# Kernel optimization log

Hardware: AMD Instinct MI355X
Metric: run time of the kernel (lower is better)

The kernel has to match this reference:

```python
import jax, jax.numpy as jnp
import numpy as np

DIM = 1024
NUM_HEADS = 16
HEAD_DIM = DIM // NUM_HEADS
SCALE = HEAD_DIM ** (-0.5)


def setup_inputs() -> dict:
    key = jax.random.key(0)
    ks = jax.random.split(key, 5)
    B, L, D = 2, 2048, DIM
    x = jax.random.normal(ks[0], (B, L, D), dtype=jnp.float32)
    # torch nn.Linear init scale ~ U(-1/sqrt(fan_in), 1/sqrt(fan_in)); use small normals
    s = 1.0 / np.sqrt(D)
    qkv_w = jax.random.uniform(ks[1], (3 * D, D), minval=-s, maxval=s, dtype=jnp.float32)
    qkv_b = jax.random.uniform(ks[2], (3 * D,), minval=-s, maxval=s, dtype=jnp.float32)
    proj_w = jax.random.uniform(ks[3], (D, D), minval=-s, maxval=s, dtype=jnp.float32)
    proj_b = jax.random.uniform(ks[4], (D,), minval=-s, maxval=s, dtype=jnp.float32)
    return {"x": x, "qkv_w": qkv_w, "qkv_b": qkv_b, "proj_w": proj_w, "proj_b": proj_b}


def reference(x, qkv_w, qkv_b, proj_w, proj_b):
    B, L, D = x.shape
    H, Hd = NUM_HEADS, HEAD_DIM
    # QKV projection: [B,L,3D] -> [3,B,H,L,Hd]
    qkv = x @ qkv_w.T + qkv_b
    qkv = qkv.reshape(B, L, 3, H, Hd).transpose(2, 0, 3, 1, 4)
    q, k, v = qkv[0], qkv[1], qkv[2]
    scores = jnp.einsum('bhqd,bhkd->bhqk', q, k) * SCALE  # [B,H,L,L]
    attn = jax.nn.softmax(scores, axis=-1)
    out = jnp.einsum('bhqk,bhkd->bhqd', attn, v)  # [B,H,L,Hd]
    out = out.transpose(0, 2, 1, 3).reshape(B, L, D)
    out = out @ proj_w.T + proj_b
    return out
```

## Files before the change

kernel.cpp:

```cpp
#include <hip/hip_runtime.h>
#include <hip/hip_bf16.h>
#include <cstdint>
#include <cstddef>

#define D_MODEL 1024
#define NHEADS 16
#define HD 64
#define NB 2
#define SL 2048
#define SEQ (NB*SL)
#define NQKV (3*D_MODEL)

typedef __attribute__((ext_vector_type(8))) short short8;
typedef __attribute__((ext_vector_type(4))) float floatx4;
typedef __attribute__((ext_vector_type(16))) float f32x16;
typedef unsigned short u16;

__device__ __forceinline__ u16 f2bf(float f) {
    union { float f; uint32_t u; } v; v.f = f;
    return (u16)((v.u + 0x7fffu + ((v.u >> 16) & 1u)) >> 16);
}

__device__ __forceinline__ uint32_t cvt_pk_bf16(float lo, float hi) {
    uint32_t r;
    asm("v_cvt_pk_bf16_f32 %0, %1, %2" : "=v"(r) : "v"(lo), "v"(hi));
    return r;
}

__device__ __forceinline__ void pl32swap(uint32_t &a, uint32_t &b) {
    asm("v_permlane32_swap_b32 %0, %1" : "+v"(a), "+v"(b));
}

__device__ __forceinline__ float exp2f_fast(float x) {
    float r; asm("v_exp_f32 %0, %1" : "=v"(r) : "v"(x)); return r;
}

__device__ __forceinline__ float m3f(float a, float b, float c) {
    return fmaxf(fmaxf(a, b), c);
}

__device__ __forceinline__ float vmax16(const f32x16& v) {
    float a0 = m3f(v[0], v[1], v[2]);
    float a1 = m3f(v[3], v[4], v[5]);
    float a2 = m3f(v[6], v[7], v[8]);
    float a3 = m3f(v[9], v[10], v[11]);
    float a4 = m3f(v[12], v[13], v[14]);
    return fmaxf(m3f(a0, a1, v[15]), m3f(a2, a3, a4));
}

__device__ __forceinline__ f32x16 zero16() {
    f32x16 z;
    #pragma unroll
    for (int i = 0; i < 16; i++) z[i] = 0.f;
    return z;
}

#define GLDS(gsrc, ldst) __builtin_amdgcn_global_load_lds( \
    (const __attribute__((address_space(1))) void*)(gsrc), \
    (__attribute__((address_space(3))) void*)(ldst), 16, 0, 0)

__global__ __launch_bounds__(256) void cvt_all(const float* __restrict__ x,
                                               const float* __restrict__ w1,
                                               const float* __restrict__ w2,
                                               u16* __restrict__ xb,
                                               u16* __restrict__ w1b,
                                               u16* __restrict__ w2b) {
    int i = blockIdx.x * 256 + threadIdx.x;
    const float4* src; ushort4* dst; int j;
    if (i < 1048576)      { src = (const float4*)x;  dst = (ushort4*)xb;  j = i; }
    else if (i < 1835008) { src = (const float4*)w1; dst = (ushort4*)w1b; j = i - 1048576; }
    else                  { src = (const float4*)w2; dst = (ushort4*)w2b; j = i - 1835008; }
    float4 f = src[j];
    ushort4 o;
    o.x = f2bf(f.x); o.y = f2bf(f.y); o.z = f2bf(f.z); o.w = f2bf(f.w);
    dst[j] = o;
}

__device__ __forceinline__ void gemm128_staged(const u16* __restrict__ A,
                                               const u16* __restrict__ B,
                                               int mbase, int nbase, int K,
                                               u16* Alds, u16* Blds,
                                               floatx4 acc[4][4]) {
    const int tid = threadIdx.x;
    const int lane = tid & 63;
    const int l15 = lane & 15, quad = lane >> 4;
    const int wave = tid >> 6;
    const int wr = wave >> 1, wc = wave & 1;
    #pragma unroll
    for (int i = 0; i < 4; i++)
        #pragma unroll
        for (int j = 0; j < 4; j++)
            acc[i][j] = (floatx4){0.f, 0.f, 0.f, 0.f};

    const int r0 = tid >> 2, kg0 = (tid & 3) * 8;
    const int r1 = (256 + tid) >> 2, kg1 = kg0;
    const u16* Arow0 = A + (size_t)(mbase + r0) * K + kg0;
    const u16* Arow1 = A + (size_t)(mbase + r1) * K + kg1;
    const u16* Brow0 = B + (size_t)(nbase + r0) * K + kg0;
    const u16* Brow1 = B + (size_t)(nbase + r1) * K + kg1;

    for (int k0 = 0; k0 < K; k0 += 32) {
        __syncthreads();
        GLDS(Arow0 + k0, Alds + tid * 8);
        GLDS(Arow1 + k0, Alds + (256 + tid) * 8);
        GLDS(Brow0 + k0, Blds + tid * 8);
        GLDS(Brow1 + k0, Blds + (256 + tid) * 8);
        __syncthreads();

        short8 af[4], bf[4];
        #pragma unroll
        for (int i = 0; i < 4; i++)
            af[i] = *(const short8*)(Alds + (wr * 64 + i * 16 + l15) * 32 + quad * 8);
        #pragma unroll
        for (int j = 0; j < 4; j++)
            bf[j] = *(const short8*)(Blds + (wc * 64 + j * 16 + l15) * 32 + quad * 8);
        #pragma unroll
        for (int i = 0; i < 4; i++)
            #pragma unroll
            for (int j = 0; j < 4; j++)
                acc[i][j] = __builtin_amdgcn_mfma_f32_16x16x32_bf16(af[i], bf[j], acc[i][j], 0, 0, 0);
    }
}

__global__ __launch_bounds__(256) void qkv_gemm(const u16* __restrict__ xb,
                                                const u16* __restrict__ wb,
                                                const float* __restrict__ bias,
                                                u16* __restrict__ Qo, u16* __restrict__ Ko,
                                                u16* __restrict__ Vt) {
    __shared__ __align__(16) u16 Alds[128 * 32];
    __shared__ __align__(16) u16 Blds[128 * 32];
    const int mbase = blockIdx.y * 128;
    const int nbase = blockIdx.x * 128;
    floatx4 acc[4][4];
    gemm128_staged(xb, wb, mbase, nbase, 1024, Alds, Blds, acc);
    const int lane = threadIdx.x & 63;
    const int wave = threadIdx.x >> 6;
    const int wr = wave >> 1, wc = wave & 1;
    const int l15 = lane & 15, quad = lane >> 4;
    #pragma unroll
    for (int j = 0; j < 4; j++) {
        int n = nbase + wc * 64 + j * 16 + l15;
        float bv = bias[n];
        int which = n >> 10;
        int within = n & 1023;
        int h = within >> 6, d = within & 63;
        #pragma unroll
        for (int i = 0; i < 4; i++) {
            #pragma unroll
            for (int r = 0; r < 4; r++) {
                int m = mbase + wr * 64 + i * 16 + quad * 4 + r;
                int b = m >> 11, l = m & 2047;
                int bh = b * NHEADS + h;
                float v = acc[i][j][r] + bv;
                if (which == 0) {
                    Qo[((size_t)bh * SL + l) * HD + d] = f2bf(v * 0.18033688f);
                } else if (which == 1) {
                    int slot = ((l >> 5) & 1) * 256 + (d >> 4) * 64 + ((d >> 3) & 1) * 32 + (l & 31);
                    Ko[(size_t)bh * (SL * HD) + (size_t)(l >> 6) * 4096 + slot * 8 + (d & 7)] = f2bf(v);
                } else {
                    int slot = ((l >> 5) & 1) * 256 + ((l >> 4) & 1) * 128 + (d >> 5) * 64 + ((l >> 3) & 1) * 32 + (d & 31);
                    Vt[(size_t)bh * (SL * HD) + (size_t)(l >> 6) * 4096 + slot * 8 + (l & 7)] = f2bf(v);
                }
            }
        }
    }
}

__global__ __launch_bounds__(256, 2) void flash_kernel(const u16* __restrict__ Q,
                                                       const u16* __restrict__ K,
                                                       const u16* __restrict__ V,
                                                       u16* __restrict__ AO) {
    __shared__ __align__(16) u16 Klds[2 * 4096];
    __shared__ __align__(16) u16 Vlds[2 * 4096];
    const int tid = threadIdx.x;
    const int lane = tid & 63;
    const int wave = tid >> 6;
    const int hi = lane >> 5;
    const int l31 = lane & 31;
    const int lane8 = lane * 8;

    const int bid = (int)blockIdx.x;
    const int swz = (bid & 7) * 64 + (bid >> 3);
    const int bh = swz >> 4;
    const int qb = swz & 15;
    const int b = bh >> 4, h = bh & 15;
    const int qbase = qb * 128 + wave * 32;

    const u16* Qp = Q + (size_t)bh * SL * HD;
    const u16* Kg = K + (size_t)bh * (SL * HD);
    const u16* Vg = V + (size_t)bh * (SL * HD);

    short8 qf[4];
    #pragma unroll
    for (int c = 0; c < 4; c++)
        qf[c] = *(const short8*)(Qp + (size_t)(qbase + l31) * HD + c * 16 + hi * 8);

    f32x16 accO0 = zero16(), accO1 = zero16();
    float m_i = -__builtin_inff();
    float l_i = 0.f;

    GLDS(Kg + tid * 8,         Klds + tid * 8);
    GLDS(Kg + (256 + tid) * 8, Klds + (256 + tid) * 8);
    GLDS(Vg + tid * 8,         Vlds + tid * 8);
    GLDS(Vg + (256 + tid) * 8, Vlds + (256 + tid) * 8);
    __syncthreads();

    union PW { uint32_t w[4]; short8 s8; };

    for (int t = 0; t < SL / 64; t++) {
        const int cur = t & 1;
        if (t + 1 < SL / 64) {
            const u16* ks = Kg + (size_t)(t + 1) * 4096;
            const u16* vs = Vg + (size_t)(t + 1) * 4096;
            u16* kd = Klds + (cur ^ 1) * 4096;
            u16* vd = Vlds + (cur ^ 1) * 4096;
            GLDS(ks + tid * 8,         kd + tid * 8);
            GLDS(ks + (256 + tid) * 8, kd + (256 + tid) * 8);
            GLDS(vs + tid * 8,         vd + tid * 8);
            GLDS(vs + (256 + tid) * 8, vd + (256 + tid) * 8);
        }
        const u16* Kt  = Klds + cur * 4096;
        const u16* Vt_ = Vlds + cur * 4096;

        f32x16 sA = zero16(), sB = zero16();
        __builtin_amdgcn_s_setprio(1);
        #pragma unroll
        for (int c = 0; c < 4; c++) {
            short8 kf = *(const short8*)(Kt + c * 512 + lane8);
            sA = __builtin_amdgcn_mfma_f32_32x32x16_bf16(kf, qf[c], sA, 0, 0, 0);
        }
        #pragma unroll
        for (int c = 0; c < 4; c++) {
            short8 kf = *(const short8*)(Kt + 2048 + c * 512 + lane8);
            sB = __builtin_amdgcn_mfma_f32_32x32x16_bf16(kf, qf[c], sB, 0, 0, 0);
        }
        __builtin_amdgcn_s_setprio(0);

        float pmax = fmaxf(vmax16(sA), vmax16(sB));
        if (!__all(pmax - m_i <= 24.0f)) {
            float mo = m_i;
            float mn = fmaxf(mo, fmaxf(pmax, __shfl_xor(pmax, 32, 64)));
            m_i = mn;
            float alpha = exp2f_fast(mo - mn);
            l_i *= alpha;
            #pragma unroll
            for (int e = 0; e < 16; e++) { accO0[e] *= alpha; accO1[e] *= alpha; }
        }
        #pragma unroll
        for (int e = 0; e < 16; e++) sA[e] = exp2f_fast(sA[e] - m_i);
        #pragma unroll
        for (int e = 0; e < 16; e++) sB[e] = exp2f_fast(sB[e] - m_i);
        float r0 = 0.f, r1 = 0.f, r2 = 0.f, r3 = 0.f;
        #pragma unroll
        for (int e = 0; e < 16; e += 4) {
            r0 += sA[e]; r1 += sA[e + 1]; r2 += sA[e + 2]; r3 += sA[e + 3];
        }
        #pragma unroll
        for (int e = 0; e < 16; e += 4) {
            r0 += sB[e]; r1 += sB[e + 1]; r2 += sB[e + 2]; r3 += sB[e + 3];
        }
        float rs = (r0 + r1) + (r2 + r3);
        rs += __shfl_xor(rs, 32, 64);
        l_i += rs;

#define PV_SUB(SV, OFF) { \
        uint32_t a0 = cvt_pk_bf16(SV[0], SV[1]);  uint32_t b0 = cvt_pk_bf16(SV[4], SV[5]);  pl32swap(a0, b0); \
        uint32_t a1 = cvt_pk_bf16(SV[2], SV[3]);  uint32_t b1 = cvt_pk_bf16(SV[6], SV[7]);  pl32swap(a1, b1); \
        PW f0; f0.w[0] = a0; f0.w[1] = a1; f0.w[2] = b0; f0.w[3] = b1; \
        accO0 = __builtin_amdgcn_mfma_f32_32x32x16_bf16(*(const short8*)(Vt_ + (OFF) + lane8),        f0.s8, accO0, 0, 0, 0); \
        accO1 = __builtin_amdgcn_mfma_f32_32x32x16_bf16(*(const short8*)(Vt_ + (OFF) + 512 + lane8),  f0.s8, accO1, 0, 0, 0); \
        uint32_t c0 = cvt_pk_bf16(SV[8], SV[9]);  uint32_t d0 = cvt_pk_bf16(SV[12], SV[13]); pl32swap(c0, d0); \
        uint32_t c1 = cvt_pk_bf16(SV[10], SV[11]); uint32_t d1 = cvt_pk_bf16(SV[14], SV[15]); pl32swap(c1, d1); \
        PW f1; f1.w[0] = c0; f1.w[1] = c1; f1.w[2] = d0; f1.w[3] = d1; \
        accO0 = __builtin_amdgcn_mfma_f32_32x32x16_bf16(*(const short8*)(Vt_ + (OFF) + 1024 + lane8),       f1.s8, accO0, 0, 0, 0); \
        accO1 = __builtin_amdgcn_mfma_f32_32x32x16_bf16(*(const short8*)(Vt_ + (OFF) + 1024 + 512 + lane8), f1.s8, accO1, 0, 0, 0); }

        __builtin_amdgcn_s_setprio(1);
        PV_SUB(sA, 0);
        PV_SUB(sB, 2048);
        __builtin_amdgcn_s_setprio(0);
#undef PV_SUB

        __syncthreads();
    }

    const float invl = 1.f / l_i;
    const int qrow = qbase + l31;
    const size_t rowbase = ((size_t)(b * SL + qrow)) * D_MODEL + h * HD;
    #pragma unroll
    for (int rg = 0; rg < 4; rg++) {
        ushort4 o0, o1;
        o0.x = f2bf(accO0[rg * 4 + 0] * invl); o0.y = f2bf(accO0[rg * 4 + 1] * invl);
        o0.z = f2bf(accO0[rg * 4 + 2] * invl); o0.w = f2bf(accO0[rg * 4 + 3] * invl);
        *(ushort4*)(AO + rowbase + rg * 8 + 4 * hi) = o0;
        o1.x = f2bf(accO1[rg * 4 + 0] * invl); o1.y = f2bf(accO1[rg * 4 + 1] * invl);
        o1.z = f2bf(accO1[rg * 4 + 2] * invl); o1.w = f2bf(accO1[rg * 4 + 3] * invl);
        *(ushort4*)(AO + rowbase + 32 + rg * 8 + 4 * hi) = o1;
    }
}

__global__ __launch_bounds__(256) void proj_gemm(const u16* __restrict__ ab,
                                                 const u16* __restrict__ wb,
                                                 const float* __restrict__ bias,
                                                 float* __restrict__ out) {
    __shared__ __align__(16) u16 Alds[128 * 32];
    __shared__ __align__(16) u16 Blds[128 * 32];
    const int mbase = blockIdx.y * 128;
    const int nbase = blockIdx.x * 128;
    floatx4 acc[4][4];
    gemm128_staged(ab, wb, mbase, nbase, 1024, Alds, Blds, acc);
    const int lane = threadIdx.x & 63;
    const int wave = threadIdx.x >> 6;
    const int wr = wave >> 1, wc = wave & 1;
    const int l15 = lane & 15, quad = lane >> 4;
    #pragma unroll
    for (int j = 0; j < 4; j++) {
        int n = nbase + wc * 64 + j * 16 + l15;
        float bv = bias[n];
        #pragma unroll
        for (int i = 0; i < 4; i++) {
            #pragma unroll
            for (int r = 0; r < 4; r++) {
                int m = mbase + wr * 64 + i * 16 + quad * 4 + r;
                out[(size_t)m * D_MODEL + n] = acc[i][j][r] + bv;
            }
        }
    }
}

extern "C" void kernel_launch(void* const* d_in, const int* in_sizes, int n_in,
                              void* d_out, int out_size, void* d_ws, size_t ws_size,
                              hipStream_t stream) {
    const float* x      = (const float*)d_in[0];
    const float* qkv_w  = (const float*)d_in[1];
    const float* qkv_b  = (const float*)d_in[2];
    const float* proj_w = (const float*)d_in[3];
    const float* proj_b = (const float*)d_in[4];
    float* out = (float*)d_out;
    char* ws = (char*)d_ws;

    u16* xb    = (u16*)(ws);
    u16* wqkv  = (u16*)(ws + 8388608);
    u16* wproj = (u16*)(ws + 14680064);
    u16* Qb    = (u16*)(ws + 16777216);
    u16* Kb    = (u16*)(ws + 25165824);
    u16* Vt    = (u16*)(ws + 33554432);
    u16* AO    = (u16*)(ws + 41943040);

    cvt_all<<<8192, 256, 0, stream>>>(x, qkv_w, proj_w, xb, wqkv, wproj);
    qkv_gemm<<<dim3(NQKV / 128, SEQ / 128), 256, 0, stream>>>(xb, wqkv, qkv_b, Qb, Kb, Vt);
    flash_kernel<<<dim3(512), 256, 0, stream>>>(Qb, Kb, Vt, AO);
    proj_gemm<<<dim3(D_MODEL / 128, SEQ / 128), 256, 0, stream>>>(AO, wproj, proj_b, out);
}
```

Before: 207.3 us.

## Double-buffer LDS staging in projection GEMMs and vectorize V-transpose stores

```diff
diff --git a/kernel.cpp b/kernel.cpp
--- a/kernel.cpp
+++ b/kernel.cpp
@@ -76,11 +76,11 @@
     dst[j] = o;
 }
 
-__device__ __forceinline__ void gemm128_staged(const u16* __restrict__ A,
-                                               const u16* __restrict__ B,
-                                               int mbase, int nbase, int K,
-                                               u16* Alds, u16* Blds,
-                                               floatx4 acc[4][4]) {
+__device__ __forceinline__ void gemm128_dbuf(const u16* __restrict__ A,
+                                             const u16* __restrict__ B,
+                                             int mbase, int nbase, int K,
+                                             u16* Alds, u16* Blds,
+                                             floatx4 acc[4][4]) {
     const int tid = threadIdx.x;
     const int lane = tid & 63;
     const int l15 = lane & 15, quad = lane >> 4;
@@ -93,32 +93,44 @@
             acc[i][j] = (floatx4){0.f, 0.f, 0.f, 0.f};
 
     const int r0 = tid >> 2, kg0 = (tid & 3) * 8;
-    const int r1 = (256 + tid) >> 2, kg1 = kg0;
     const u16* Arow0 = A + (size_t)(mbase + r0) * K + kg0;
-    const u16* Arow1 = A + (size_t)(mbase + r1) * K + kg1;
+    const u16* Arow1 = A + (size_t)(mbase + r0 + 64) * K + kg0;
     const u16* Brow0 = B + (size_t)(nbase + r0) * K + kg0;
-    const u16* Brow1 = B + (size_t)(nbase + r1) * K + kg1;
-
-    for (int k0 = 0; k0 < K; k0 += 32) {
-        __syncthreads();
-        GLDS(Arow0 + k0, Alds + tid * 8);
-        GLDS(Arow1 + k0, Alds + (256 + tid) * 8);
-        GLDS(Brow0 + k0, Blds + tid * 8);
-        GLDS(Brow1 + k0, Blds + (256 + tid) * 8);
-        __syncthreads();
-
+    const u16* Brow1 = B + (size_t)(nbase + r0 + 64) * K + kg0;
+
+    GLDS(Arow0, Alds + tid * 8);
+    GLDS(Arow1, Alds + (256 + tid) * 8);
+    GLDS(Brow0, Blds + tid * 8);
+    GLDS(Brow1, Blds + (256 + tid) * 8);
+    __syncthreads();
+
+    const int NT = K >> 5;
+    for (int t = 0; t < NT; t++) {
+        const int cur = t & 1;
+        if (t + 1 < NT) {
+            const int k0 = (t + 1) << 5;
+            u16* Ad = Alds + (cur ^ 1) * 4096;
+            u16* Bd = Blds + (cur ^ 1) * 4096;
+            GLDS(Arow0 + k0, Ad + tid * 8);
+            GLDS(Arow1 + k0, Ad + (256 + tid) * 8);
+            GLDS(Brow0 + k0, Bd + tid * 8);
+            GLDS(Brow1 + k0, Bd + (256 + tid) * 8);
+        }
+        const u16* Ac = Alds + cur * 4096;
+        const u16* Bc = Blds + cur * 4096;
         short8 af[4], bf[4];
         #pragma unroll
         for (int i = 0; i < 4; i++)
-            af[i] = *(const short8*)(Alds + (wr * 64 + i * 16 + l15) * 32 + quad * 8);
+            af[i] = *(const short8*)(Ac + (wr * 64 + i * 16 + l15) * 32 + quad * 8);
         #pragma unroll
         for (int j = 0; j < 4; j++)
-            bf[j] = *(const short8*)(Blds + (wc * 64 + j * 16 + l15) * 32 + quad * 8);
+            bf[j] = *(const short8*)(Bc + (wc * 64 + j * 16 + l15) * 32 + quad * 8);
         #pragma unroll
         for (int i = 0; i < 4; i++)
             #pragma unroll
             for (int j = 0; j < 4; j++)
                 acc[i][j] = __builtin_amdgcn_mfma_f32_16x16x32_bf16(af[i], bf[j], acc[i][j], 0, 0, 0);
+        __syncthreads();
     }
 }
 
@@ -127,39 +139,47 @@
                                                 const float* __restrict__ bias,
                                                 u16* __restrict__ Qo, u16* __restrict__ Ko,
                                                 u16* __restrict__ Vt) {
-    __shared__ __align__(16) u16 Alds[128 * 32];
-    __shared__ __align__(16) u16 Blds[128 * 32];
+    __shared__ __align__(16) u16 Alds[2 * 128 * 32];
+    __shared__ __align__(16) u16 Blds[2 * 128 * 32];
     const int mbase = blockIdx.y * 128;
     const int nbase = blockIdx.x * 128;
     floatx4 acc[4][4];
-    gemm128_staged(xb, wb, mbase, nbase, 1024, Alds, Blds, acc);
+    gemm128_dbuf(xb, wb, mbase, nbase, 1024, Alds, Blds, acc);
     const int lane = threadIdx.x & 63;
     const int wave = threadIdx.x >> 6;
     const int wr = wave >> 1, wc = wave & 1;
     const int l15 = lane & 15, quad = lane >> 4;
+    const int which = nbase >> 10;
     #pragma unroll
     for (int j = 0; j < 4; j++) {
         int n = nbase + wc * 64 + j * 16 + l15;
         float bv = bias[n];
-        int which = n >> 10;
         int within = n & 1023;
         int h = within >> 6, d = within & 63;
         #pragma unroll
         for (int i = 0; i < 4; i++) {
-            #pragma unroll
-            for (int r = 0; r < 4; r++) {
-                int m = mbase + wr * 64 + i * 16 + quad * 4 + r;
-                int b = m >> 11, l = m & 2047;
-                int bh = b * NHEADS + h;
-                float v = acc[i][j][r] + bv;
-                if (which == 0) {
-                    Qo[((size_t)bh * SL + l) * HD + d] = f2bf(v * 0.18033688f);
-                } else if (which == 1) {
-                    int slot = ((l >> 5) & 1) * 256 + (d >> 4) * 64 + ((d >> 3) & 1) * 32 + (l & 31);
-                    Ko[(size_t)bh * (SL * HD) + (size_t)(l >> 6) * 4096 + slot * 8 + (d & 7)] = f2bf(v);
-                } else {
-                    int slot = ((l >> 5) & 1) * 256 + ((l >> 4) & 1) * 128 + (d >> 5) * 64 + ((l >> 3) & 1) * 32 + (d & 31);
-                    Vt[(size_t)bh * (SL * HD) + (size_t)(l >> 6) * 4096 + slot * 8 + (l & 7)] = f2bf(v);
+            int m0 = mbase + wr * 64 + i * 16 + quad * 4;
+            int b = m0 >> 11;
+            int bh = b * NHEADS + h;
+            if (which == 2) {
+                int l0 = m0 & 2047;
+                int slot = ((l0 >> 5) & 1) * 256 + ((l0 >> 4) & 1) * 128 + (d >> 5) * 64 + ((l0 >> 3) & 1) * 32 + (d & 31);
+                ushort4 pk;
+                pk.x = f2bf(acc[i][j][0] + bv); pk.y = f2bf(acc[i][j][1] + bv);
+                pk.z = f2bf(acc[i][j][2] + bv); pk.w = f2bf(acc[i][j][3] + bv);
+                *(ushort4*)(Vt + (size_t)bh * (SL * HD) + (size_t)(l0 >> 6) * 4096 + slot * 8 + (l0 & 7)) = pk;
+            } else {
+                #pragma unroll
+                for (int r = 0; r < 4; r++) {
+                    int m = m0 + r;
+                    int l = m & 2047;
+                    float v = acc[i][j][r] + bv;
+                    if (which == 0) {
+                        Qo[((size_t)bh * SL + l) * HD + d] = f2bf(v * 0.18033688f);
+                    } else {
+                        int slot = ((l >> 5) & 1) * 256 + (d >> 4) * 64 + ((d >> 3) & 1) * 32 + (l & 31);
+                        Ko[(size_t)bh * (SL * HD) + (size_t)(l >> 6) * 4096 + slot * 8 + (d & 7)] = f2bf(v);
+                    }
                 }
             }
         }
@@ -303,12 +323,12 @@
                                                  const u16* __restrict__ wb,
                                                  const float* __restrict__ bias,
                                                  float* __restrict__ out) {
-    __shared__ __align__(16) u16 Alds[128 * 32];
-    __shared__ __align__(16) u16 Blds[128 * 32];
+    __shared__ __align__(16) u16 Alds[2 * 128 * 32];
+    __shared__ __align__(16) u16 Blds[2 * 128 * 32];
     const int mbase = blockIdx.y * 128;
     const int nbase = blockIdx.x * 128;
     floatx4 acc[4][4];
-    gemm128_staged(ab, wb, mbase, nbase, 1024, Alds, Blds, acc);
+    gemm128_dbuf(ab, wb, mbase, nbase, 1024, Alds, Blds, acc);
     const int lane = threadIdx.x & 63;
     const int wave = threadIdx.x >> 6;
     const int wr = wave >> 1, wc = wave & 1;
```

Result: faster. 198.6 us (-4.2%).
